# Performance work log

Hardware: AMD Instinct MI355X
Metric: run time of the kernel (lower is better)

Reference implementation:

```python
import jax, jax.numpy as jnp
import numpy as np

KERNEL = 4
OUT_C = 64


def setup_inputs() -> dict:
    key = jax.random.key(0)
    k1, k2 = jax.random.split(key)
    x = jax.random.normal(k1, (64, 256, 28, 28), dtype=jnp.float32)
    # per-location unshared weights: [h*w, in_c, out_c*k*k]
    weight = jax.random.normal(k2, (28 * 28, 256, OUT_C * KERNEL * KERNEL), dtype=jnp.float32)
    return {"x": x, "weight": weight}


def reference(x, weight):
    bs, c, h, w = x.shape
    k = KERNEL
    oc = OUT_C
    # locally-connected matmul: for each spatial location l, x[b,:,l] @ weight[l]
    patches = jnp.einsum('bcl,lcd->bld', x.reshape(bs, c, h * w), weight)  # [bs, hw, oc*k*k]
    # torch Fold layout: channel dim ordered as (oc, kh, kw)
    patches = patches.reshape(bs, h, w, oc, k, k)
    H, W = h + k - 1, w + k - 1  # fold with stride=1 (nn.Fold default)
    out = jnp.zeros((bs, oc, H, W), dtype=x.dtype)
    # overlap-add: k*k static shifted accumulations
    for di in range(k):
        for dj in range(k):
            out = out.at[:, :, di:di + h, dj:dj + w].add(
                patches[:, :, :, :, di, dj].transpose(0, 3, 1, 2))
    return out
```

## Files before the change

### kernel.cpp

```cpp
#include <hip/hip_runtime.h>
#include <hip/hip_bf16.h>

#define HW_   784
#define C_IN  256
#define BS    64
#define OC_   64
#define D_TOT 1024
#define OH_   31
#define OW_   31

typedef __attribute__((ext_vector_type(8))) short    short8;
typedef __attribute__((ext_vector_type(4))) float    f32x4;
typedef __attribute__((ext_vector_type(4))) int      int4v;
typedef __attribute__((ext_vector_type(4))) _Float16 half4;

static __device__ __forceinline__ short f2bf(float f) {
    unsigned int u = __float_as_uint(f);
    unsigned int r = (u + 0x7fffu + ((u >> 16) & 1u)) >> 16;
    return (short)r;
}

__global__ __launch_bounds__(256) void pack_x(const float* __restrict__ x,
                                              __hip_bfloat16* __restrict__ xp) {
    const int b  = blockIdx.x;
    const int c0 = blockIdx.y * 32;
    const int l0 = blockIdx.z * 112;
    const int t  = threadIdx.x;

    __shared__ unsigned short tile[32][114];

    for (int e = t; e < 32 * 112; e += 256) {
        int cl = e / 112, ll = e % 112;
        float v = x[(size_t)b * (C_IN * HW_) + (size_t)(c0 + cl) * HW_ + (l0 + ll)];
        tile[cl][ll] = (unsigned short)f2bf(v);
    }
    __syncthreads();

    for (int e = t; e < 112 * 32; e += 256) {
        int ll = e >> 5, cl = e & 31;
        xp[(size_t)(l0 + ll) * (BS * C_IN) + b * C_IN + (c0 + cl)] =
            *(const __hip_bfloat16*)&tile[cl][ll];
    }
}

__global__ __launch_bounds__(256) void lc_gemm(const __hip_bfloat16* __restrict__ xp,
                                               const float* __restrict__ W,
                                               _Float16* __restrict__ patches) {
    const int wg   = blockIdx.x;
    const int lcid = (wg & 7) * 392 + (wg >> 3);
    const int l     = lcid >> 2;
    const int chunk = lcid & 3;

    const int t     = threadIdx.x;
    const int wave  = t >> 6;
    const int lane  = t & 63;
    const int g     = lane >> 4;
    const int ln    = lane & 15;

    __shared__ int4v alds4[2048];
    char* alds = (char*)alds4;

    {
        const int4v* src = (const int4v*)(xp + (size_t)l * (BS * C_IN));
        #pragma unroll
        for (int it = 0; it < 8; ++it) {
            int ch  = t + it * 256;
            int row = ch >> 5;
            int col = ch & 31;
            int4v v = src[ch];
            *(int4v*)(alds + row * 512 + ((col * 16) ^ ((row & 7) << 4))) = v;
        }
    }
    __syncthreads();

    const float* Wl    = W + (size_t)l * (C_IN * D_TOT);
    const int    dbase = chunk * 256 + wave * 64;

    f32x4 acc[4][4];
    #pragma unroll
    for (int m = 0; m < 4; ++m)
        #pragma unroll
        for (int n = 0; n < 4; ++n)
            acc[m][n] = (f32x4){0.f, 0.f, 0.f, 0.f};

    for (int k0 = 0; k0 < C_IN; k0 += 32) {
        float wv[4][8];
        #pragma unroll
        for (int n = 0; n < 4; ++n) {
            const float* p = Wl + (size_t)(k0 + g * 8) * D_TOT + (dbase + 16 * n + ln);
            #pragma unroll
            for (int tt = 0; tt < 8; ++tt) wv[n][tt] = p[(size_t)tt * D_TOT];
        }

        short8 af[4];
        #pragma unroll
        for (int m = 0; m < 4; ++m) {
            int row = 16 * m + ln;
            int off = row * 512 + ((((k0 + g * 8) << 1)) ^ ((row & 7) << 4));
            af[m] = *(const short8*)(alds + off);
        }

        short8 bf[4];
        #pragma unroll
        for (int n = 0; n < 4; ++n)
            #pragma unroll
            for (int tt = 0; tt < 8; ++tt) bf[n][tt] = f2bf(wv[n][tt]);

        #pragma unroll
        for (int m = 0; m < 4; ++m)
            #pragma unroll
            for (int n = 0; n < 4; ++n)
                acc[m][n] = __builtin_amdgcn_mfma_f32_16x16x32_bf16(af[m], bf[n],
                                                                   acc[m][n], 0, 0, 0);
    }

    __syncthreads();
    _Float16* hl = (_Float16*)alds;
    #pragma unroll
    for (int m = 0; m < 4; ++m) {
        #pragma unroll
        for (int n = 0; n < 4; ++n) {
            #pragma unroll
            for (int r = 0; r < 4; ++r) {
                int b  = 16 * m + g * 4 + r;
                int dp = wave * 64 + 16 * n + ln;
                hl[b * 256 + dp] = (_Float16)acc[m][n][r];
            }
        }
    }
    __syncthreads();

    _Float16* dst = patches + (size_t)l * (BS * D_TOT) + chunk * 256;
    #pragma unroll
    for (int it = 0; it < 8; ++it) {
        int idx = t + it * 256;
        int row = idx >> 5;
        int gg  = idx & 31;
        *(int4v*)(dst + (size_t)row * D_TOT + gg * 8) =
            *(const int4v*)(hl + row * 256 + gg * 8);
    }
}

__global__ __launch_bounds__(256) void fold_k(const _Float16* __restrict__ patches,
                                              float* __restrict__ out) {
    const int b   = blockIdx.x;
    const int oh0 = blockIdx.y * 4;
    const int t   = threadIdx.x;
    const int oc  = t >> 2;
    const int ww  = t & 3;
    const int wb  = ww * 8;

    float acc[4][8];
    #pragma unroll
    for (int a = 0; a < 4; ++a)
        #pragma unroll
        for (int o = 0; o < 8; ++o) acc[a][o] = 0.f;

    const size_t pboc = (size_t)b * D_TOT + (size_t)oc * 16;

    #pragma unroll
    for (int a = 0; a < 4; ++a) {
        const int oh = oh0 + a;
        if (oh > 30) continue;
        #pragma unroll
        for (int di = 0; di < 4; ++di) {
            const int r = oh - di;
            if (r < 0 || r >= 28) continue;
            #pragma unroll
            for (int k = 0; k < 11; ++k) {
                const int wp = wb - 3 + k;
                if (wp < 0 || wp >= 28) continue;
                const int l = r * 28 + wp;
                half4 v = *(const half4*)(patches + (size_t)l * (BS * D_TOT) + pboc + di * 4);
                #pragma unroll
                for (int dj = 0; dj < 4; ++dj) {
                    const int o = (k - 3) + dj;
                    if (o < 0 || o >= 8) continue;
                    if (wb + o <= 30)
                        acc[a][o] += (float)v[dj];
                }
            }
        }
    }

    #pragma unroll
    for (int a = 0; a < 4; ++a) {
        const int oh = oh0 + a;
        if (oh > 30) continue;
        float* op = out + (((size_t)b * OC_ + oc) * OH_ + oh) * OW_ + wb;
        #pragma unroll
        for (int o = 0; o < 8; ++o) {
            if (wb + o <= 30) op[o] = acc[a][o];
        }
    }
}

extern "C" void kernel_launch(void* const* d_in, const int* in_sizes, int n_in,
                              void* d_out, int out_size, void* d_ws, size_t ws_size,
                              hipStream_t stream) {
    const float* x = (const float*)d_in[0];
    const float* W = (const float*)d_in[1];
    float* out     = (float*)d_out;

    __hip_bfloat16* xp = (__hip_bfloat16*)d_ws;
    _Float16* patches  = (_Float16*)((char*)d_ws + 25690112);

    pack_x<<<dim3(64, 8, 7), 256, 0, stream>>>(x, xp);
    lc_gemm<<<dim3(HW_ * 4), 256, 0, stream>>>(xp, W, patches);
    fold_k<<<dim3(64, 8), 256, 0, stream>>>(patches, out);
}
```

Before: 265.5 us.

## Stage weights through double-buffered LDS with vectorized float4 global loads

Weight loads in the GEMM now use coalesced float4 global reads, one k-slab per wave. The values are converted to bf16 and written into a swizzled, double-buffered LDS tile, and the MFMA B fragments are read back from LDS. The next slab's global load is issued before the current slab's MFMAs to overlap memory latency with compute. The aim is to replace the scalar strided per-lane loads of the memory-bound weight stream. In exchange, LDS grows to 64KB per block, which may reduce occupancy, and a barrier is added every k-step.

```diff
diff --git a/kernel.cpp b/kernel.cpp
--- a/kernel.cpp
+++ b/kernel.cpp
@@ -12,6 +12,7 @@
 typedef __attribute__((ext_vector_type(8))) short    short8;
 typedef __attribute__((ext_vector_type(4))) float    f32x4;
 typedef __attribute__((ext_vector_type(4))) int      int4v;
+typedef __attribute__((ext_vector_type(4))) float    fl4;
 typedef __attribute__((ext_vector_type(4))) _Float16 half4;
 
 static __device__ __forceinline__ short f2bf(float f) {
@@ -46,8 +47,8 @@
 __global__ __launch_bounds__(256) void lc_gemm(const __hip_bfloat16* __restrict__ xp,
                                                const float* __restrict__ W,
                                                _Float16* __restrict__ patches) {
-    const int wg   = blockIdx.x;
-    const int lcid = (wg & 7) * 392 + (wg >> 3);
+    const int wg    = blockIdx.x;
+    const int lcid  = (wg & 7) * 392 + (wg >> 3);
     const int l     = lcid >> 2;
     const int chunk = lcid & 3;
 
@@ -57,8 +58,9 @@
     const int g     = lane >> 4;
     const int ln    = lane & 15;
 
-    __shared__ int4v alds4[2048];
-    char* alds = (char*)alds4;
+    __shared__ __attribute__((aligned(16))) char lds[64 * 1024];
+    char* alds = lds;
+    char* wlds = lds + 32 * 1024;
 
     {
         const int4v* src = (const int4v*)(xp + (size_t)l * (BS * C_IN));
@@ -71,10 +73,27 @@
             *(int4v*)(alds + row * 512 + ((col * 16) ^ ((row & 7) << 4))) = v;
         }
     }
+
+    const int kg = wave;
+    const int dg = lane;
+    const float* Wbase = W + (size_t)l * (C_IN * D_TOT) + chunk * 256 + dg * 4;
+    const int wswz = (dg & 3) << 4;
+
+    fl4 wreg[8];
+
+    #pragma unroll
+    for (int r = 0; r < 8; ++r)
+        wreg[r] = *(const fl4*)(Wbase + (size_t)(kg * 8 + r) * D_TOT);
+    #pragma unroll
+    for (int j = 0; j < 4; ++j) {
+        short8 pk;
+        #pragma unroll
+        for (int r = 0; r < 8; ++r) pk[r] = f2bf(wreg[r][j]);
+        *(short8*)(wlds + (4 * dg + j) * 64 + ((kg * 16) ^ wswz)) = pk;
+    }
     __syncthreads();
 
-    const float* Wl    = W + (size_t)l * (C_IN * D_TOT);
-    const int    dbase = chunk * 256 + wave * 64;
+    const int dbase = chunk * 256 + wave * 64;
 
     f32x4 acc[4][4];
     #pragma unroll
@@ -83,13 +102,22 @@
         for (int n = 0; n < 4; ++n)
             acc[m][n] = (f32x4){0.f, 0.f, 0.f, 0.f};
 
-    for (int k0 = 0; k0 < C_IN; k0 += 32) {
-        float wv[4][8];
+    for (int s = 0; s < 8; ++s) {
+        char* wcur = wlds + (s & 1) * 16384;
+        char* wnxt = wlds + ((s & 1) ^ 1) * 16384;
+        const int k0 = s * 32;
+
+        if (s < 7) {
+            #pragma unroll
+            for (int r = 0; r < 8; ++r)
+                wreg[r] = *(const fl4*)(Wbase + (size_t)(k0 + 32 + kg * 8 + r) * D_TOT);
+        }
+
+        short8 bfr[4];
         #pragma unroll
         for (int n = 0; n < 4; ++n) {
-            const float* p = Wl + (size_t)(k0 + g * 8) * D_TOT + (dbase + 16 * n + ln);
-            #pragma unroll
-            for (int tt = 0; tt < 8; ++tt) wv[n][tt] = p[(size_t)tt * D_TOT];
+            int dl = wave * 64 + 16 * n + ln;
+            bfr[n] = *(const short8*)(wcur + dl * 64 + ((g * 16) ^ ((ln >> 2) << 4)));
         }
 
         short8 af[4];
@@ -100,21 +128,25 @@
             af[m] = *(const short8*)(alds + off);
         }
 
-        short8 bf[4];
-        #pragma unroll
-        for (int n = 0; n < 4; ++n)
-            #pragma unroll
-            for (int tt = 0; tt < 8; ++tt) bf[n][tt] = f2bf(wv[n][tt]);
-
         #pragma unroll
         for (int m = 0; m < 4; ++m)
             #pragma unroll
             for (int n = 0; n < 4; ++n)
-                acc[m][n] = __builtin_amdgcn_mfma_f32_16x16x32_bf16(af[m], bf[n],
+                acc[m][n] = __builtin_amdgcn_mfma_f32_16x16x32_bf16(af[m], bfr[n],
                                                                    acc[m][n], 0, 0, 0);
-    }
-
-    __syncthreads();
+
+        if (s < 7) {
+            #pragma unroll
+            for (int j = 0; j < 4; ++j) {
+                short8 pk;
+                #pragma unroll
+                for (int r = 0; r < 8; ++r) pk[r] = f2bf(wreg[r][j]);
+                *(short8*)(wnxt + (4 * dg + j) * 64 + ((kg * 16) ^ wswz)) = pk;
+            }
+        }
+        __syncthreads();
+    }
+
     _Float16* hl = (_Float16*)alds;
     #pragma unroll
     for (int m = 0; m < 4; ++m) {
```

Measured after the change: 262.6 us. No clear change (-1.1%).

## Switch GEMM to fp16 MFMA with vectorized, double-buffered weight prefetch

Applied to the files above, without the earlier changes.

Replaces the bf16 inputs and manual rounding with fp16 conversion and fp16 MFMA. Weight loads change from scalar strided floats to float4 loads per lane, with columns remapped so each lane owns 4 consecutive outputs. Two register buffers prefetch the next K slab while the current one computes, to hide the latency of the dominant weight read. The epilogue writes half4 vectors to LDS. The cost is more registers, and fp16 has less range than bf16.

```diff
diff --git a/kernel.cpp b/kernel.cpp
--- a/kernel.cpp
+++ b/kernel.cpp
@@ -9,45 +9,39 @@
 #define OH_   31
 #define OW_   31
 
-typedef __attribute__((ext_vector_type(8))) short    short8;
+typedef __attribute__((ext_vector_type(8))) _Float16 half8;
+typedef __attribute__((ext_vector_type(4))) _Float16 half4;
 typedef __attribute__((ext_vector_type(4))) float    f32x4;
+typedef __attribute__((ext_vector_type(4))) float    fl4;
 typedef __attribute__((ext_vector_type(4))) int      int4v;
-typedef __attribute__((ext_vector_type(4))) _Float16 half4;
-
-static __device__ __forceinline__ short f2bf(float f) {
-    unsigned int u = __float_as_uint(f);
-    unsigned int r = (u + 0x7fffu + ((u >> 16) & 1u)) >> 16;
-    return (short)r;
-}
 
 __global__ __launch_bounds__(256) void pack_x(const float* __restrict__ x,
-                                              __hip_bfloat16* __restrict__ xp) {
+                                              _Float16* __restrict__ xp) {
     const int b  = blockIdx.x;
     const int c0 = blockIdx.y * 32;
     const int l0 = blockIdx.z * 112;
     const int t  = threadIdx.x;
 
-    __shared__ unsigned short tile[32][114];
+    __shared__ _Float16 tile[32][114];
 
     for (int e = t; e < 32 * 112; e += 256) {
         int cl = e / 112, ll = e % 112;
         float v = x[(size_t)b * (C_IN * HW_) + (size_t)(c0 + cl) * HW_ + (l0 + ll)];
-        tile[cl][ll] = (unsigned short)f2bf(v);
+        tile[cl][ll] = (_Float16)v;
     }
     __syncthreads();
 
     for (int e = t; e < 112 * 32; e += 256) {
         int ll = e >> 5, cl = e & 31;
-        xp[(size_t)(l0 + ll) * (BS * C_IN) + b * C_IN + (c0 + cl)] =
-            *(const __hip_bfloat16*)&tile[cl][ll];
-    }
-}
-
-__global__ __launch_bounds__(256) void lc_gemm(const __hip_bfloat16* __restrict__ xp,
+        xp[(size_t)(l0 + ll) * (BS * C_IN) + b * C_IN + (c0 + cl)] = tile[cl][ll];
+    }
+}
+
+__global__ __launch_bounds__(256) void lc_gemm(const _Float16* __restrict__ xp,
                                                const float* __restrict__ W,
                                                _Float16* __restrict__ patches) {
-    const int wg   = blockIdx.x;
-    const int lcid = (wg & 7) * 392 + (wg >> 3);
+    const int wg    = blockIdx.x;
+    const int lcid  = (wg & 7) * 392 + (wg >> 3);
     const int l     = lcid >> 2;
     const int chunk = lcid & 3;
 
@@ -57,8 +51,7 @@
     const int g     = lane >> 4;
     const int ln    = lane & 15;
 
-    __shared__ int4v alds4[2048];
-    char* alds = (char*)alds4;
+    __shared__ __attribute__((aligned(16))) char lds[32 * 1024];
 
     {
         const int4v* src = (const int4v*)(xp + (size_t)l * (BS * C_IN));
@@ -68,13 +61,20 @@
             int row = ch >> 5;
             int col = ch & 31;
             int4v v = src[ch];
-            *(int4v*)(alds + row * 512 + ((col * 16) ^ ((row & 7) << 4))) = v;
-        }
-    }
-    __syncthreads();
-
-    const float* Wl    = W + (size_t)l * (C_IN * D_TOT);
-    const int    dbase = chunk * 256 + wave * 64;
+            *(int4v*)(lds + row * 512 + ((col * 16) ^ ((row & 7) << 4))) = v;
+        }
+    }
+    __syncthreads();
+
+    const float* Wb = W + (size_t)l * (C_IN * D_TOT) + chunk * 256 + wave * 64 + 4 * ln;
+
+    fl4 wA[8], wB[8];
+    #pragma unroll
+    for (int r = 0; r < 8; ++r)
+        wA[r] = *(const fl4*)(Wb + (size_t)(g * 8 + r) * D_TOT);
+    #pragma unroll
+    for (int r = 0; r < 8; ++r)
+        wB[r] = *(const fl4*)(Wb + (size_t)(32 + g * 8 + r) * D_TOT);
 
     f32x4 acc[4][4];
     #pragma unroll
@@ -83,49 +83,77 @@
         for (int n = 0; n < 4; ++n)
             acc[m][n] = (f32x4){0.f, 0.f, 0.f, 0.f};
 
-    for (int k0 = 0; k0 < C_IN; k0 += 32) {
-        float wv[4][8];
-        #pragma unroll
-        for (int n = 0; n < 4; ++n) {
-            const float* p = Wl + (size_t)(k0 + g * 8) * D_TOT + (dbase + 16 * n + ln);
-            #pragma unroll
-            for (int tt = 0; tt < 8; ++tt) wv[n][tt] = p[(size_t)tt * D_TOT];
-        }
-
-        short8 af[4];
-        #pragma unroll
-        for (int m = 0; m < 4; ++m) {
-            int row = 16 * m + ln;
-            int off = row * 512 + ((((k0 + g * 8) << 1)) ^ ((row & 7) << 4));
-            af[m] = *(const short8*)(alds + off);
-        }
-
-        short8 bf[4];
-        #pragma unroll
-        for (int n = 0; n < 4; ++n)
-            #pragma unroll
-            for (int tt = 0; tt < 8; ++tt) bf[n][tt] = f2bf(wv[n][tt]);
-
-        #pragma unroll
-        for (int m = 0; m < 4; ++m)
+    #pragma unroll
+    for (int s = 0; s < 8; s += 2) {
+        {
+            half8 bfr[4];
             #pragma unroll
             for (int n = 0; n < 4; ++n)
-                acc[m][n] = __builtin_amdgcn_mfma_f32_16x16x32_bf16(af[m], bf[n],
-                                                                   acc[m][n], 0, 0, 0);
-    }
-
-    __syncthreads();
-    _Float16* hl = (_Float16*)alds;
+                #pragma unroll
+                for (int tt = 0; tt < 8; ++tt) bfr[n][tt] = (_Float16)wA[tt][n];
+
+            if (s + 2 < 8) {
+                #pragma unroll
+                for (int r = 0; r < 8; ++r)
+                    wA[r] = *(const fl4*)(Wb + (size_t)((s + 2) * 32 + g * 8 + r) * D_TOT);
+            }
+
+            const int k0 = s * 32;
+            half8 af[4];
+            #pragma unroll
+            for (int m = 0; m < 4; ++m) {
+                int row = 16 * m + ln;
+                af[m] = *(const half8*)(lds + row * 512 +
+                                        ((((k0 + g * 8) << 1)) ^ ((row & 7) << 4)));
+            }
+            #pragma unroll
+            for (int m = 0; m < 4; ++m)
+                #pragma unroll
+                for (int n = 0; n < 4; ++n)
+                    acc[m][n] = __builtin_amdgcn_mfma_f32_16x16x32_f16(af[m], bfr[n],
+                                                                       acc[m][n], 0, 0, 0);
+        }
+        {
+            half8 bfr[4];
+            #pragma unroll
+            for (int n = 0; n < 4; ++n)
+                #pragma unroll
+                for (int tt = 0; tt < 8; ++tt) bfr[n][tt] = (_Float16)wB[tt][n];
+
+            if (s + 3 < 8) {
+                #pragma unroll
+                for (int r = 0; r < 8; ++r)
+                    wB[r] = *(const fl4*)(Wb + (size_t)((s + 3) * 32 + g * 8 + r) * D_TOT);
+            }
+
+            const int k0 = (s + 1) * 32;
+            half8 af[4];
+            #pragma unroll
+            for (int m = 0; m < 4; ++m) {
+                int row = 16 * m + ln;
+                af[m] = *(const half8*)(lds + row * 512 +
+                                        ((((k0 + g * 8) << 1)) ^ ((row & 7) << 4)));
+            }
+            #pragma unroll
+            for (int m = 0; m < 4; ++m)
+                #pragma unroll
+                for (int n = 0; n < 4; ++n)
+                    acc[m][n] = __builtin_amdgcn_mfma_f32_16x16x32_f16(af[m], bfr[n],
+                                                                       acc[m][n], 0, 0, 0);
+        }
+    }
+
+    __syncthreads();
+    _Float16* hl = (_Float16*)lds;
     #pragma unroll
     for (int m = 0; m < 4; ++m) {
         #pragma unroll
-        for (int n = 0; n < 4; ++n) {
-            #pragma unroll
-            for (int r = 0; r < 4; ++r) {
-                int b  = 16 * m + g * 4 + r;
-                int dp = wave * 64 + 16 * n + ln;
-                hl[b * 256 + dp] = (_Float16)acc[m][n][r];
-            }
+        for (int r = 0; r < 4; ++r) {
+            int b = 16 * m + 4 * g + r;
+            half4 hq;
+            #pragma unroll
+            for (int n = 0; n < 4; ++n) hq[n] = (_Float16)acc[m][n][r];
+            *(half4*)(hl + b * 256 + wave * 64 + 4 * ln) = hq;
         }
     }
     __syncthreads();
@@ -202,8 +230,8 @@
     const float* W = (const float*)d_in[1];
     float* out     = (float*)d_out;
 
-    __hip_bfloat16* xp = (__hip_bfloat16*)d_ws;
-    _Float16* patches  = (_Float16*)((char*)d_ws + 25690112);
+    _Float16* xp      = (_Float16*)d_ws;
+    _Float16* patches = (_Float16*)((char*)d_ws + 25690112);
 
     pack_x<<<dim3(64, 8, 7), 256, 0, stream>>>(x, xp);
     lc_gemm<<<dim3(HW_ * 4), 256, 0, stream>>>(xp, W, patches);
```

New measurement: 270.6 us. About the same (+2.0%).
